# Kernel optimization log

Hardware: AMD Instinct MI355X
Metric: run time of the kernel (lower is better)

The kernel has to match this reference:

```python
import jax, jax.numpy as jnp
import numpy as np

B, S, DIM = 2, 2048, 4096
HQ, HKV, HD = 32, 8, 128
N_REP = HQ // HKV
MAX_S = 2048
ROPE_BASE = 10000.0


def rotate_half(x):
    half = x.shape[-1] // 2
    return jnp.concatenate([-x[..., half:], x[..., :half]], axis=-1)


def setup_inputs() -> dict:
    key = jax.random.key(0)
    ks = jax.random.split(key, 8)
    x = jax.random.normal(ks[0], (B, S, DIM), dtype=jnp.float32)
    Wq = jax.random.normal(ks[1], (HQ * HD, DIM), dtype=jnp.float32) * 0.02
    bq = jax.random.normal(ks[2], (HQ * HD,), dtype=jnp.float32) * 0.02
    Wk = jax.random.normal(ks[3], (HKV * HD, DIM), dtype=jnp.float32) * 0.02
    bk = jax.random.normal(ks[4], (HKV * HD,), dtype=jnp.float32) * 0.02
    Wv = jax.random.normal(ks[5], (HKV * HD, DIM), dtype=jnp.float32) * 0.02
    bv = jax.random.normal(ks[6], (HKV * HD,), dtype=jnp.float32) * 0.02
    Wo = jax.random.normal(ks[7], (DIM, HQ * HD), dtype=jnp.float32) * 0.02
    # RoPE tables (HF convention: angles duplicated across both halves)
    inv_freq = 1.0 / (ROPE_BASE ** (jnp.arange(0, HD, 2, dtype=jnp.float32) / HD))
    pos = jnp.arange(S, dtype=jnp.float32)
    ang = pos[:, None] * inv_freq[None, :]              # [S, HD/2]
    emb = jnp.concatenate([ang, ang], axis=-1)          # [S, HD]
    cos, sin = jnp.cos(emb), jnp.sin(emb)
    # static KV cache, zero-initialized as in the module
    cache_k = jnp.zeros((B, HKV, MAX_S, HD), dtype=jnp.float32)
    cache_v = jnp.zeros((B, HKV, MAX_S, HD), dtype=jnp.float32)
    # causal additive mask
    causal = jnp.tril(jnp.ones((S, S), dtype=bool))
    mask = jnp.where(causal, 0.0, -1e9).astype(jnp.float32)[None, None]  # [1,1,S,S]
    return {"x": x, "cos": cos, "sin": sin, "Wq": Wq, "bq": bq, "Wk": Wk,
            "bk": bk, "Wv": Wv, "bv": bv, "Wo": Wo, "cache_k": cache_k,
            "cache_v": cache_v, "mask": mask, "start_pos": 0}


def reference(x, cos, sin, Wq, bq, Wk, bk, Wv, bv, Wo, cache_k, cache_v, mask, start_pos):
    bsz, seqlen, _ = x.shape
    scaling = 1.0 / jnp.sqrt(jnp.float32(HD))
    # QKV projections
    xq = (jnp.einsum('bsd,ed->bse', x, Wq) + bq).reshape(bsz, seqlen, HQ, HD).transpose(0, 2, 1, 3)
    xk = (jnp.einsum('bsd,ed->bse', x, Wk) + bk).reshape(bsz, seqlen, HKV, HD).transpose(0, 2, 1, 3)
    xv = (jnp.einsum('bsd,ed->bse', x, Wv) + bv).reshape(bsz, seqlen, HKV, HD).transpose(0, 2, 1, 3)
    # RoPE
    c = cos[None, None]  # [1,1,S,HD]
    s = sin[None, None]
    xq = xq * c + rotate_half(xq) * s
    xk = xk * c + rotate_half(xk) * s
    # static KV-cache append + slice (start_pos is a Python int)
    cache_k = jax.lax.dynamic_update_slice(cache_k, xk, (0, 0, start_pos, 0))
    cache_v = jax.lax.dynamic_update_slice(cache_v, xv, (0, 0, start_pos, 0))
    keys = cache_k[:, :, :start_pos + seqlen]     # [B,HKV,K,HD]
    values = cache_v[:, :, :start_pos + seqlen]
    # GQA: repeat kv heads (repeat_interleave over head dim)
    keys = jnp.repeat(keys, N_REP, axis=1)        # [B,HQ,K,HD]
    values = jnp.repeat(values, N_REP, axis=1)
    # SDPA with additive mask
    scores = jnp.einsum('bhqd,bhkd->bhqk', xq, keys) * scaling + mask
    attn = jax.nn.softmax(scores, axis=-1)
    out = jnp.einsum('bhqk,bhkd->bhqd', attn, values)
    out = out.transpose(0, 2, 1, 3).reshape(bsz, seqlen, HQ * HD)
    return jnp.einsum('bse,de->bsd', out, Wo)
```

## Files before the change

kernel.cpp:

```cpp
#include <hip/hip_runtime.h>

typedef _Float16 half8 __attribute__((ext_vector_type(8)));
typedef _Float16 half4 __attribute__((ext_vector_type(4)));
typedef float floatx4 __attribute__((ext_vector_type(4)));
typedef float floatx16 __attribute__((ext_vector_type(16)));

#define SWZ(r) ((((r) & 7) << 1) | (((r) >> 3) & 1))

__device__ __forceinline__ void gld16(const void* g, void* l) {
  __builtin_amdgcn_global_load_lds(
      (const __attribute__((address_space(1))) unsigned int*)g,
      (__attribute__((address_space(3))) unsigned int*)l, 16, 0, 0);
}

__global__ void f2h(const float* __restrict__ s, _Float16* __restrict__ d, int n8) {
  int i = blockIdx.x * 256 + threadIdx.x;
  if (i >= n8) return;
  float4 a = ((const float4*)s)[2 * i];
  float4 b = ((const float4*)s)[2 * i + 1];
  half8 h;
  h[0] = (_Float16)a.x; h[1] = (_Float16)a.y; h[2] = (_Float16)a.z; h[3] = (_Float16)a.w;
  h[4] = (_Float16)b.x; h[5] = (_Float16)b.y; h[6] = (_Float16)b.z; h[7] = (_Float16)b.w;
  ((half8*)d)[i] = h;
}

__global__ void bias_concat(const float* __restrict__ bq, const float* __restrict__ bk,
                            const float* __restrict__ bv, float* __restrict__ dst) {
  int i = blockIdx.x * 256 + threadIdx.x;
  if (i < 4096) dst[i] = bq[i];
  else if (i < 5120) dst[i] = bk[i - 4096];
  else if (i < 6144) dst[i] = bv[i - 5120];
}

template <typename OutT, bool HasBias>
__global__ __launch_bounds__(256) void gemm_bt(const _Float16* __restrict__ A,
                                               const _Float16* __restrict__ B,
                                               const float* __restrict__ bias,
                                               OutT* __restrict__ C, int M, int N, int K) {
  __shared__ _Float16 as[128 * 32];
  __shared__ _Float16 bs[128 * 32];
  const int tid = threadIdx.x;
  const int w = tid >> 6, lane = tid & 63;
  const int quad = lane >> 4, l16 = lane & 15;
  const int M0 = blockIdx.y * 128, N0 = blockIdx.x * 128;
  const int wm = (w >> 1) * 64, wn = (w & 1) * 64;

  floatx4 acc[4][4];
#pragma unroll
  for (int i = 0; i < 4; ++i)
#pragma unroll
    for (int j = 0; j < 4; ++j) acc[i][j] = (floatx4){0.f, 0.f, 0.f, 0.f};

  const int r0 = tid >> 2, g0 = tid & 3;
  const int r1 = r0 + 64;
  const int c0 = (g0 ^ ((r0 >> 1) & 3)) * 8;
  const int c1 = (g0 ^ ((r1 >> 1) & 3)) * 8;
  const _Float16* A0 = A + (size_t)(M0 + r0) * K + c0;
  const _Float16* A1 = A + (size_t)(M0 + r1) * K + c1;
  const _Float16* B0 = B + (size_t)(N0 + r0) * K + c0;
  const _Float16* B1 = B + (size_t)(N0 + r1) * K + c1;
  _Float16* asw = &as[w * 512];
  _Float16* bsw = &bs[w * 512];

  int aoff[4], boff[4];
#pragma unroll
  for (int mi = 0; mi < 4; ++mi) {
    int ra = wm + mi * 16 + l16;
    aoff[mi] = ra * 32 + ((quad ^ ((ra >> 1) & 3)) * 8);
    int rb = wn + mi * 16 + l16;
    boff[mi] = rb * 32 + ((quad ^ ((rb >> 1) & 3)) * 8);
  }

  for (int kk = 0; kk < K; kk += 32) {
    __syncthreads();
    gld16(A0 + kk, asw);
    gld16(A1 + kk, asw + 2048);
    gld16(B0 + kk, bsw);
    gld16(B1 + kk, bsw + 2048);
    __syncthreads();
    half8 af[4], bf[4];
#pragma unroll
    for (int i = 0; i < 4; ++i) af[i] = *(const half8*)&as[aoff[i]];
#pragma unroll
    for (int i = 0; i < 4; ++i) bf[i] = *(const half8*)&bs[boff[i]];
#pragma unroll
    for (int mi = 0; mi < 4; ++mi)
#pragma unroll
      for (int ni = 0; ni < 4; ++ni)
        acc[mi][ni] = __builtin_amdgcn_mfma_f32_16x16x32_f16(af[mi], bf[ni], acc[mi][ni], 0, 0, 0);
  }

#pragma unroll
  for (int mi = 0; mi < 4; ++mi)
#pragma unroll
    for (int ni = 0; ni < 4; ++ni) {
      int row = M0 + wm + mi * 16 + quad * 4;
      int col = N0 + wn + ni * 16 + l16;
      float bvv = HasBias ? bias[col] : 0.f;
#pragma unroll
      for (int r = 0; r < 4; ++r) {
        float v = acc[mi][ni][r] + bvv;
        C[(size_t)(row + r) * N + col] = (OutT)v;
      }
    }
}

__global__ void rope_qk(const _Float16* __restrict__ qkv, const float* __restrict__ cosb,
                        const float* __restrict__ sinb, _Float16* __restrict__ q_r,
                        _Float16* __restrict__ k_r) {
  int t = blockIdx.x * 256 + threadIdx.x;
  int d = t & 63;
  int r = t >> 6;
  int hh = r % 40;
  int r2 = r / 40;
  int s = r2 & 2047;
  int b = r2 >> 11;
  size_t mrow = (size_t)(b * 2048 + s) * 6144;
  float c = cosb[s * 128 + d], sn = sinb[s * 128 + d];
  if (hh < 32) {
    size_t base = mrow + hh * 128 + d;
    float x1 = (float)qkv[base], x2 = (float)qkv[base + 64];
    const float sc = 0.12751744737079736f;
    float o1 = (x1 * c - x2 * sn) * sc;
    float o2 = (x2 * c + x1 * sn) * sc;
    size_t ob = ((size_t)((b * 32 + hh) * 2048 + s)) * 128 + d;
    q_r[ob] = (_Float16)o1;
    q_r[ob + 64] = (_Float16)o2;
  } else {
    int hk = hh - 32;
    size_t base = mrow + 4096 + hk * 128 + d;
    float x1 = (float)qkv[base], x2 = (float)qkv[base + 64];
    float o1 = x1 * c - x2 * sn;
    float o2 = x2 * c + x1 * sn;
    size_t ob = ((size_t)((b * 8 + hk) * 2048 + s)) * 128 + d;
    k_r[ob] = (_Float16)o1;
    k_r[ob + 64] = (_Float16)o2;
  }
}

__global__ void v_transpose(const _Float16* __restrict__ qkv, _Float16* __restrict__ v_t) {
  __shared__ _Float16 tile[32][33];
  int st = blockIdx.x * 32, dt = blockIdx.y * 32, bh = blockIdx.z;
  int tx = threadIdx.x & 31, ty = threadIdx.x >> 5;
  int b = bh >> 3, hv = bh & 7;
#pragma unroll
  for (int j = 0; j < 4; ++j) {
    int s = st + ty + j * 8;
    tile[ty + j * 8][tx] = qkv[(size_t)(b * 2048 + s) * 6144 + 5120 + hv * 128 + dt + tx];
  }
  __syncthreads();
#pragma unroll
  for (int j = 0; j < 4; ++j)
    v_t[((size_t)bh * 128 + dt + ty + j * 8) * 2048 + st + tx] = tile[tx][ty + j * 8];
}

__global__ __launch_bounds__(256, 2) void attn_kernel(const _Float16* __restrict__ q_r,
                                                      const _Float16* __restrict__ k_r,
                                                      const _Float16* __restrict__ v_t,
                                                      _Float16* __restrict__ att) {
  __shared__ __align__(16) _Float16 kt[128 * 128];
  __shared__ __align__(16) _Float16 vt[128 * 128];
  const int tid = threadIdx.x;
  const int w = tid >> 6, lane = tid & 63;
  const int l32 = lane & 31, hi = lane >> 5;
  const int qb = 15 - blockIdx.x;
  const int h = blockIdx.y, b = blockIdx.z;
  const int q0 = qb * 128;
  const _Float16* qh = q_r + ((size_t)(b * 32 + h) * 2048) * 128;
  const _Float16* kh = k_r + ((size_t)(b * 8 + (h >> 2)) * 2048) * 128;
  const _Float16* vh = v_t + ((size_t)(b * 8 + (h >> 2)) * 128) * 2048;

  const int ql = w * 32 + l32;
  const int myq = q0 + ql;
  const int swq = SWZ(ql);
  const int swl = SWZ(l32);

  half8 bq[8];
#pragma unroll
  for (int kd = 0; kd < 8; ++kd)
    bq[kd] = *(const half8*)&qh[(size_t)myq * 128 + kd * 16 + hi * 8];

  floatx16 oacc[4];
#pragma unroll
  for (int di = 0; di < 4; ++di)
#pragma unroll
    for (int j = 0; j < 16; ++j) oacc[di][j] = 0.f;
  float mrun = -1e30f, lrun = 0.f;

  const int srow0 = tid >> 4, sgrp = tid & 15;

  for (int kti = 0; kti <= qb; ++kti) {
    __syncthreads();
    const _Float16* kg = kh + (size_t)kti * 128 * 128;
#pragma unroll
    for (int c = 0; c < 8; ++c) {
      int row = srow0 + c * 16;
      int gc = (sgrp ^ SWZ(row)) * 8;
      gld16(kg + row * 128 + gc, &kt[w * 512 + c * 2048]);
    }
#pragma unroll
    for (int c = 0; c < 8; ++c) {
      int row = srow0 + c * 16;
      int gc = (sgrp ^ SWZ(row)) * 8;
      gld16(vh + (size_t)row * 2048 + kti * 128 + gc, &vt[w * 512 + c * 2048]);
    }
    __syncthreads();

    floatx16 sacc[4];
#pragma unroll
    for (int ni = 0; ni < 4; ++ni)
#pragma unroll
      for (int j = 0; j < 16; ++j) sacc[ni][j] = 0.f;
#pragma unroll
    for (int ni = 0; ni < 4; ++ni) {
      int rb = (ni * 32 + l32) * 128;
#pragma unroll
      for (int kd = 0; kd < 8; ++kd) {
        half8 ka = *(const half8*)&kt[rb + (((kd * 2 + hi) ^ swl) * 8)];
        sacc[ni] = __builtin_amdgcn_mfma_f32_32x32x16_f16(ka, bq[kd], sacc[ni], 0, 0, 0);
      }
    }

    if (kti == qb) {
#pragma unroll
      for (int ni = 0; ni < 4; ++ni)
#pragma unroll
        for (int g = 0; g < 4; ++g) {
          int kvb = kti * 128 + ni * 32 + g * 8 + hi * 4;
#pragma unroll
          for (int t = 0; t < 4; ++t)
            if (kvb + t > myq) sacc[ni][g * 4 + t] = -1e30f;
        }
    }

    float tm = -1e30f;
#pragma unroll
    for (int ni = 0; ni < 4; ++ni)
#pragma unroll
      for (int j = 0; j < 16; ++j) tm = fmaxf(tm, sacc[ni][j]);
    tm = fmaxf(tm, __shfl_xor(tm, 32));
    float nm = fmaxf(mrun, tm);
    float al = exp2f(mrun - nm);
    mrun = nm;
    float ts = 0.f;
#pragma unroll
    for (int ni = 0; ni < 4; ++ni)
#pragma unroll
      for (int j = 0; j < 16; ++j) {
        float p = exp2f(sacc[ni][j] - nm);
        sacc[ni][j] = p;
        ts += p;
      }
    ts += __shfl_xor(ts, 32);
    lrun = lrun * al + ts;
#pragma unroll
    for (int di = 0; di < 4; ++di)
#pragma unroll
      for (int j = 0; j < 16; ++j) oacc[di][j] *= al;

    __syncthreads();

#pragma unroll
    for (int ni = 0; ni < 4; ++ni)
#pragma unroll
      for (int g = 0; g < 4; ++g) {
        half4 p4;
#pragma unroll
        for (int t = 0; t < 4; ++t) p4[t] = (_Float16)sacc[ni][g * 4 + t];
        *(half4*)&kt[ql * 128 + (((ni * 4 + g) ^ swq) * 8) + hi * 4] = p4;
      }

#pragma unroll
    for (int ks = 0; ks < 8; ++ks) {
      half8 pb = *(const half8*)&kt[ql * 128 + (((ks * 2 + hi) ^ swq) * 8)];
#pragma unroll
      for (int di = 0; di < 4; ++di) {
        int rv = (di * 32 + l32) * 128;
        half8 va = *(const half8*)&vt[rv + (((ks * 2 + hi) ^ swl) * 8)];
        oacc[di] = __builtin_amdgcn_mfma_f32_32x32x16_f16(va, pb, oacc[di], 0, 0, 0);
      }
    }
  }

  float inv = 1.f / lrun;
  _Float16* ob = att + ((size_t)b * 2048 + myq) * 4096 + h * 128;
#pragma unroll
  for (int di = 0; di < 4; ++di)
#pragma unroll
    for (int g = 0; g < 4; ++g) {
      half4 o4;
#pragma unroll
      for (int t = 0; t < 4; ++t) o4[t] = (_Float16)(oacc[di][g * 4 + t] * inv);
      *(half4*)&ob[di * 32 + g * 8 + hi * 4] = o4;
    }
}

extern "C" void kernel_launch(void* const* d_in, const int* in_sizes, int n_in, void* d_out,
                              int out_size, void* d_ws, size_t ws_size, hipStream_t stream) {
  const float* x = (const float*)d_in[0];
  const float* cosb = (const float*)d_in[1];
  const float* sinb = (const float*)d_in[2];
  const float* Wq = (const float*)d_in[3];
  const float* bq = (const float*)d_in[4];
  const float* Wk = (const float*)d_in[5];
  const float* bk = (const float*)d_in[6];
  const float* Wv = (const float*)d_in[7];
  const float* bv = (const float*)d_in[8];
  const float* Wo = (const float*)d_in[9];
  float* out = (float*)d_out;

  char* p = (char*)d_ws;
  _Float16* xb = (_Float16*)p;   p += (size_t)4096 * 4096 * 2;
  _Float16* wqkv = (_Float16*)p; p += (size_t)6144 * 4096 * 2;
  _Float16* wo_b = (_Float16*)p; p += (size_t)4096 * 4096 * 2;
  _Float16* qkv = (_Float16*)p;  p += (size_t)4096 * 6144 * 2;
  _Float16* q_r = (_Float16*)p;  p += (size_t)2 * 32 * 2048 * 128 * 2;
  _Float16* k_r = (_Float16*)p;  p += (size_t)2 * 8 * 2048 * 128 * 2;
  _Float16* v_t = (_Float16*)p;  p += (size_t)2 * 8 * 128 * 2048 * 2;
  _Float16* att = (_Float16*)p;  p += (size_t)4096 * 4096 * 2;
  float* biasc = (float*)p;      p += 6144 * 4;

  f2h<<<8192, 256, 0, stream>>>(x, xb, 2097152);
  f2h<<<8192, 256, 0, stream>>>(Wq, wqkv, 2097152);
  f2h<<<2048, 256, 0, stream>>>(Wk, wqkv + (size_t)4096 * 4096, 524288);
  f2h<<<2048, 256, 0, stream>>>(Wv, wqkv + (size_t)5120 * 4096, 524288);
  f2h<<<8192, 256, 0, stream>>>(Wo, wo_b, 2097152);
  bias_concat<<<24, 256, 0, stream>>>(bq, bk, bv, biasc);

  gemm_bt<_Float16, true><<<dim3(48, 32), 256, 0, stream>>>(xb, wqkv, biasc, qkv, 4096, 6144, 4096);
  rope_qk<<<40960, 256, 0, stream>>>(qkv, cosb, sinb, q_r, k_r);
  v_transpose<<<dim3(64, 4, 16), 256, 0, stream>>>(qkv, v_t);
  attn_kernel<<<dim3(16, 32, 2), 256, 0, stream>>>(q_r, k_r, v_t, att);
  gemm_bt<float, false><<<dim3(32, 32), 256, 0, stream>>>(att, wo_b, nullptr, out, 4096, 4096, 4096);
}
```

Before: 951.9 us.

## Fuse fp32-to-fp16 conversions into one launch and double GEMM K-tile to 64

The five f2h launches and the bias concat are merged into a single convert_all kernel, which removes several kernel launches. The GEMM now stages 64-wide K tiles in shared memory using an 8-way XOR swizzle and runs two MFMA sub-steps per tile, so there are half as many syncthreads barriers per unit of work. In exchange, shared memory per block doubles and the converter's branch logic is more complex.

```diff
diff --git a/kernel.cpp b/kernel.cpp
--- a/kernel.cpp
+++ b/kernel.cpp
@@ -13,23 +13,36 @@
       (__attribute__((address_space(3))) unsigned int*)l, 16, 0, 0);
 }
 
-__global__ void f2h(const float* __restrict__ s, _Float16* __restrict__ d, int n8) {
-  int i = blockIdx.x * 256 + threadIdx.x;
-  if (i >= n8) return;
-  float4 a = ((const float4*)s)[2 * i];
-  float4 b = ((const float4*)s)[2 * i + 1];
+__global__ void convert_all(const float* __restrict__ x, const float* __restrict__ Wq,
+                            const float* __restrict__ Wk, const float* __restrict__ Wv,
+                            const float* __restrict__ Wo, const float* __restrict__ bq,
+                            const float* __restrict__ bk, const float* __restrict__ bv,
+                            _Float16* __restrict__ xb, _Float16* __restrict__ wqkv,
+                            _Float16* __restrict__ wo_b, float* __restrict__ biasc) {
+  long i = (long)blockIdx.x * 256 + threadIdx.x;
+  const long N0 = 2097152, N1 = N0 + 2097152, N2 = N1 + 524288, N3 = N2 + 524288,
+             N4 = N3 + 2097152;
+  const float* s;
+  _Float16* d;
+  long j;
+  if (i < N0) { s = x; d = xb; j = i; }
+  else if (i < N1) { s = Wq; d = wqkv; j = i - N0; }
+  else if (i < N2) { s = Wk; d = wqkv + (size_t)4096 * 4096; j = i - N1; }
+  else if (i < N3) { s = Wv; d = wqkv + (size_t)5120 * 4096; j = i - N2; }
+  else if (i < N4) { s = Wo; d = wo_b; j = i - N3; }
+  else {
+    long k = i - N4;
+    if (k < 4096) biasc[k] = bq[k];
+    else if (k < 5120) biasc[k] = bk[k - 4096];
+    else if (k < 6144) biasc[k] = bv[k - 5120];
+    return;
+  }
+  float4 a = ((const float4*)s)[2 * j];
+  float4 b2 = ((const float4*)s)[2 * j + 1];
   half8 h;
   h[0] = (_Float16)a.x; h[1] = (_Float16)a.y; h[2] = (_Float16)a.z; h[3] = (_Float16)a.w;
-  h[4] = (_Float16)b.x; h[5] = (_Float16)b.y; h[6] = (_Float16)b.z; h[7] = (_Float16)b.w;
-  ((half8*)d)[i] = h;
-}
-
-__global__ void bias_concat(const float* __restrict__ bq, const float* __restrict__ bk,
-                            const float* __restrict__ bv, float* __restrict__ dst) {
-  int i = blockIdx.x * 256 + threadIdx.x;
-  if (i < 4096) dst[i] = bq[i];
-  else if (i < 5120) dst[i] = bk[i - 4096];
-  else if (i < 6144) dst[i] = bv[i - 5120];
+  h[4] = (_Float16)b2.x; h[5] = (_Float16)b2.y; h[6] = (_Float16)b2.z; h[7] = (_Float16)b2.w;
+  ((half8*)d)[j] = h;
 }
 
 template <typename OutT, bool HasBias>
@@ -37,8 +50,8 @@
                                                const _Float16* __restrict__ B,
                                                const float* __restrict__ bias,
                                                OutT* __restrict__ C, int M, int N, int K) {
-  __shared__ _Float16 as[128 * 32];
-  __shared__ _Float16 bs[128 * 32];
+  __shared__ _Float16 as[128 * 64];
+  __shared__ _Float16 bs[128 * 64];
   const int tid = threadIdx.x;
   const int w = tid >> 6, lane = tid & 63;
   const int quad = lane >> 4, l16 = lane & 15;
@@ -51,43 +64,51 @@
 #pragma unroll
     for (int j = 0; j < 4; ++j) acc[i][j] = (floatx4){0.f, 0.f, 0.f, 0.f};
 
-  const int r0 = tid >> 2, g0 = tid & 3;
-  const int r1 = r0 + 64;
-  const int c0 = (g0 ^ ((r0 >> 1) & 3)) * 8;
-  const int c1 = (g0 ^ ((r1 >> 1) & 3)) * 8;
-  const _Float16* A0 = A + (size_t)(M0 + r0) * K + c0;
-  const _Float16* A1 = A + (size_t)(M0 + r1) * K + c1;
-  const _Float16* B0 = B + (size_t)(N0 + r0) * K + c0;
-  const _Float16* B1 = B + (size_t)(N0 + r1) * K + c1;
-  _Float16* asw = &as[w * 512];
-  _Float16* bsw = &bs[w * 512];
-
-  int aoff[4], boff[4];
-#pragma unroll
-  for (int mi = 0; mi < 4; ++mi) {
-    int ra = wm + mi * 16 + l16;
-    aoff[mi] = ra * 32 + ((quad ^ ((ra >> 1) & 3)) * 8);
-    int rb = wn + mi * 16 + l16;
-    boff[mi] = rb * 32 + ((quad ^ ((rb >> 1) & 3)) * 8);
-  }
-
-  for (int kk = 0; kk < K; kk += 32) {
-    __syncthreads();
-    gld16(A0 + kk, asw);
-    gld16(A1 + kk, asw + 2048);
-    gld16(B0 + kk, bsw);
-    gld16(B1 + kk, bsw + 2048);
-    __syncthreads();
-    half8 af[4], bf[4];
-#pragma unroll
-    for (int i = 0; i < 4; ++i) af[i] = *(const half8*)&as[aoff[i]];
-#pragma unroll
-    for (int i = 0; i < 4; ++i) bf[i] = *(const half8*)&bs[boff[i]];
-#pragma unroll
-    for (int mi = 0; mi < 4; ++mi)
-#pragma unroll
-      for (int ni = 0; ni < 4; ++ni)
-        acc[mi][ni] = __builtin_amdgcn_mfma_f32_16x16x32_f16(af[mi], bf[ni], acc[mi][ni], 0, 0, 0);
+  const int sr = tid >> 3, g0 = tid & 7;
+  const int csw = (g0 ^ (sr & 7)) * 8;
+  const _Float16* Ag[4];
+  const _Float16* Bg[4];
+  _Float16* asd[4];
+  _Float16* bsd[4];
+#pragma unroll
+  for (int c = 0; c < 4; ++c) {
+    Ag[c] = A + (size_t)(M0 + c * 32 + sr) * K + csw;
+    Bg[c] = B + (size_t)(N0 + c * 32 + sr) * K + csw;
+    asd[c] = &as[(c * 32 + w * 8) * 64];
+    bsd[c] = &bs[(c * 32 + w * 8) * 64];
+  }
+
+  int aoff[4][2], boff[4][2];
+#pragma unroll
+  for (int mi = 0; mi < 4; ++mi)
+#pragma unroll
+    for (int kd = 0; kd < 2; ++kd) {
+      int ra = wm + mi * 16 + l16;
+      aoff[mi][kd] = ra * 64 + (((kd * 4 + quad) ^ (ra & 7)) * 8);
+      int rb = wn + mi * 16 + l16;
+      boff[mi][kd] = rb * 64 + (((kd * 4 + quad) ^ (rb & 7)) * 8);
+    }
+
+  for (int kk = 0; kk < K; kk += 64) {
+    __syncthreads();
+#pragma unroll
+    for (int c = 0; c < 4; ++c) gld16(Ag[c] + kk, asd[c]);
+#pragma unroll
+    for (int c = 0; c < 4; ++c) gld16(Bg[c] + kk, bsd[c]);
+    __syncthreads();
+#pragma unroll
+    for (int kd = 0; kd < 2; ++kd) {
+      half8 af[4], bf[4];
+#pragma unroll
+      for (int i = 0; i < 4; ++i) af[i] = *(const half8*)&as[aoff[i][kd]];
+#pragma unroll
+      for (int i = 0; i < 4; ++i) bf[i] = *(const half8*)&bs[boff[i][kd]];
+#pragma unroll
+      for (int mi = 0; mi < 4; ++mi)
+#pragma unroll
+        for (int ni = 0; ni < 4; ++ni)
+          acc[mi][ni] = __builtin_amdgcn_mfma_f32_16x16x32_f16(af[mi], bf[ni], acc[mi][ni], 0, 0, 0);
+    }
   }
 
 #pragma unroll
@@ -320,12 +341,7 @@
   _Float16* att = (_Float16*)p;  p += (size_t)4096 * 4096 * 2;
   float* biasc = (float*)p;      p += 6144 * 4;
 
-  f2h<<<8192, 256, 0, stream>>>(x, xb, 2097152);
-  f2h<<<8192, 256, 0, stream>>>(Wq, wqkv, 2097152);
-  f2h<<<2048, 256, 0, stream>>>(Wk, wqkv + (size_t)4096 * 4096, 524288);
-  f2h<<<2048, 256, 0, stream>>>(Wv, wqkv + (size_t)5120 * 4096, 524288);
-  f2h<<<8192, 256, 0, stream>>>(Wo, wo_b, 2097152);
-  bias_concat<<<24, 256, 0, stream>>>(bq, bk, bv, biasc);
+  convert_all<<<28696, 256, 0, stream>>>(x, Wq, Wk, Wv, Wo, bq, bk, bv, xb, wqkv, wo_b, biasc);
 
   gemm_bt<_Float16, true><<<dim3(48, 32), 256, 0, stream>>>(xb, wqkv, biasc, qkv, 4096, 6144, 4096);
   rope_qk<<<40960, 256, 0, stream>>>(qkv, cosb, sinb, q_r, k_r);
```

Result: faster. 896.3 us (-5.8%).
